# Kernel optimization log

Hardware: AMD Instinct MI355X
Metric: run time of the kernel (lower is better)

## Reference

```python
import jax, jax.numpy as jnp
import numpy as np

B, C, H, W = 4, 256, 64, 64
E = C // 8  # embedding_channels = inChannels // k


def setup_inputs() -> dict:
    key = jax.random.key(0)
    ks = jax.random.split(key, 9)
    sc = 1.0 / np.sqrt(C)
    so = 1.0 / np.sqrt(E)
    return {
        "x": jax.random.normal(ks[0], (B, C, H, W), dtype=jnp.float32),
        "Wk": jax.random.normal(ks[1], (E, C), dtype=jnp.float32) * sc,
        "bk": jax.random.normal(ks[2], (E,), dtype=jnp.float32) * 0.01,
        "Wq": jax.random.normal(ks[3], (E, C), dtype=jnp.float32) * sc,
        "bq": jax.random.normal(ks[4], (E,), dtype=jnp.float32) * 0.01,
        "Wv": jax.random.normal(ks[5], (E, C), dtype=jnp.float32) * sc,
        "bv": jax.random.normal(ks[6], (E,), dtype=jnp.float32) * 0.01,
        "Wo": jax.random.normal(ks[7], (C, E), dtype=jnp.float32) * so,
        "bo": jax.random.normal(ks[8], (C,), dtype=jnp.float32) * 0.01,
    }


def reference(x, Wk, bk, Wq, bq, Wv, bv, Wo, bo):
    b, c, h, w = x.shape
    n = h * w
    gamma = jnp.float32(0.5)  # non-learned branch (learned=False default)

    def conv1x1(inp, Wt, bt):
        # 1x1 conv == channel-mixing matmul: [b,c,h,w] x [e,c] -> [b,e,h,w]
        return jnp.einsum('bchw,ec->behw', inp, Wt) + bt[None, :, None, None]

    f = conv1x1(x, Wk, bk).reshape(b, -1, n)  # key   [b,E,N]
    g = conv1x1(x, Wq, bq).reshape(b, -1, n)  # query [b,E,N]
    hx = conv1x1(x, Wv, bv).reshape(b, -1, n)  # value [b,E,N]

    s = jnp.einsum('bei,bej->bij', f, g)       # f^T @ g, [b,N,N]
    beta = jax.nn.softmax(s, axis=1)           # softmax over dim 1 (rows) as in torch
    v = jnp.einsum('bei,bij->bej', hx, beta)   # h @ beta, [b,E,N]
    v = v.reshape(b, -1, h, w)

    o = jnp.einsum('behw,ce->bchw', v, Wo) + bo[None, :, None, None]
    y = gamma * o + x
    return y, o, gamma
```

## Files before the change

kernel.cpp:

```cpp
#include <hip/hip_runtime.h>

#define B_ 4
#define C_ 256
#define N_ 4096
#define E_ 32

typedef _Float16 f16x8 __attribute__((ext_vector_type(8)));
typedef _Float16 f16x4 __attribute__((ext_vector_type(4)));
typedef float f32x4 __attribute__((ext_vector_type(4)));

#define LOG2E 1.44269504088896f

#define XSWZ(row, col) ((col) ^ ((((row) >> 2) & 7) << 3))

__global__ __launch_bounds__(256) void proj_kernel(
    const float* __restrict__ x,
    const float* __restrict__ Wk, const float* __restrict__ bk,
    const float* __restrict__ Wq, const float* __restrict__ bq,
    const float* __restrict__ Wv, const float* __restrict__ bv,
    const float* __restrict__ Wo,
    _Float16* __restrict__ Qb, _Float16* __restrict__ Kb, _Float16* __restrict__ Vb,
    _Float16* __restrict__ Wof16, float* __restrict__ out)
{
    const int m = blockIdx.x >> 8;
    if (m == 3) {
        for (int i4 = threadIdx.x; i4 < (C_ * E_) / 4; i4 += 256) {
            float4 wv = ((const float4*)Wo)[i4];
            f16x4 tp = {(_Float16)wv.x, (_Float16)wv.y, (_Float16)wv.z, (_Float16)wv.w};
            *(f16x4*)&Wof16[i4 * 4] = tp;
        }
        if (threadIdx.x == 0)
            out[(size_t)2 * B_ * C_ * N_] = 0.5f;
        return;
    }
    const int rem = blockIdx.x & 255;
    const int b   = rem >> 6;
    const int n0  = (rem & 63) << 6;
    const int t    = threadIdx.x;
    const int lane = t & 63;
    const int wave = t >> 6;
    const int l15  = lane & 15;
    const int quad = lane >> 4;

    __shared__ _Float16 xT[64][264];
    __shared__ _Float16 Wl[32][264];

    const float* W    = (m == 0) ? Wk : (m == 1) ? Wq : Wv;
    const float* bias = (m == 0) ? bk : (m == 1) ? bq : bv;

    for (int i4 = t; i4 < (E_ * C_) / 4; i4 += 256) {
        float4 wv = ((const float4*)W)[i4];
        int e = (i4 * 4) >> 8, c = (i4 * 4) & 255;
        f16x4 tp = {(_Float16)wv.x, (_Float16)wv.y, (_Float16)wv.z, (_Float16)wv.w};
        *(f16x4*)&Wl[e][c] = tp;
    }
    for (int i4 = t; i4 < (64 * 256) / 4; i4 += 256) {
        int j4 = (i4 & 15) * 4;
        int c  = i4 >> 4;
        float4 xv = *(const float4*)(x + (size_t)(b * C_ + c) * N_ + n0 + j4);
        xT[j4 + 0][XSWZ(j4 + 0, c)] = (_Float16)xv.x;
        xT[j4 + 1][XSWZ(j4 + 1, c)] = (_Float16)xv.y;
        xT[j4 + 2][XSWZ(j4 + 2, c)] = (_Float16)xv.z;
        xT[j4 + 3][XSWZ(j4 + 3, c)] = (_Float16)xv.w;
    }
    __syncthreads();

    const int row = wave * 16 + l15;
    f16x8 Bf[8];
    for (int kk = 0; kk < 8; ++kk)
        Bf[kk] = *(const f16x8*)&xT[row][XSWZ(row, kk * 32 + quad * 8)];

    const float sc = (m == 1) ? LOG2E : 1.0f;
    for (int et = 0; et < 2; ++et) {
        f32x4 acc = {0.f, 0.f, 0.f, 0.f};
        for (int kk = 0; kk < 8; ++kk) {
            f16x8 Af = *(const f16x8*)&Wl[et * 16 + l15][kk * 32 + quad * 8];
            acc = __builtin_amdgcn_mfma_f32_16x16x32_f16(Af, Bf[kk], acc, 0, 0, 0);
        }
        const int n  = n0 + wave * 16 + l15;
        const int e0 = et * 16 + quad * 4;
        if (m == 2) {
            for (int r = 0; r < 4; ++r)
                Vb[(size_t)(b * E_ + e0 + r) * N_ + n] =
                    (_Float16)(acc[r] + bias[e0 + r]);
        } else {
            f16x4 st;
            for (int r = 0; r < 4; ++r)
                st[r] = (_Float16)((acc[r] + bias[e0 + r]) * sc);
            _Float16* dst = (m == 0) ? Kb : Qb;
            *(f16x4*)&dst[(size_t)(b * N_ + n) * E_ + e0] = st;
        }
    }
}

__global__ __launch_bounds__(512, 6) void attn_kernel(
    const _Float16* __restrict__ Qb, const _Float16* __restrict__ Kb,
    const _Float16* __restrict__ Vb, const _Float16* __restrict__ Wof16,
    const float* __restrict__ bo, const float* __restrict__ x,
    float* __restrict__ out)
{
    const int wave = threadIdx.x >> 6;
    const int lane = threadIdx.x & 63;
    const int l15  = lane & 15, quad = lane >> 4;
    const int jg   = blockIdx.x;
    const int b    = jg >> 8;
    const int j0   = (jg & 255) << 4;

    __shared__ __align__(16) char pbuf[8][2176];
    __shared__ float    mls[8][2][16];
    __shared__ _Float16 Om[16][40];

    _Float16 (*pb)[40] = (_Float16 (*)[40])(pbuf[wave]);

    f16x8 Qf = *(const f16x8*)(Qb + (size_t)(b * N_ + j0 + l15) * E_ + quad * 8);

    f32x4 O0 = {0, 0, 0, 0}, O1 = {0, 0, 0, 0};
    float mrow = -1e30f, lsum = 0.f;

    const _Float16* Kp = Kb + (size_t)b * N_ * E_ + (size_t)(wave << 9) * E_;
    const _Float16* Vp = Vb + (size_t)b * E_ * N_ + (wave << 9);

    f16x8 K0 = *(const f16x8*)(Kp + (size_t)l15 * E_ + quad * 8);
    f16x8 K1 = *(const f16x8*)(Kp + (size_t)(16 + l15) * E_ + quad * 8);
    f16x8 Va = *(const f16x8*)(Vp + (size_t)l15 * N_ + quad * 8);
    f16x8 Vc = *(const f16x8*)(Vp + (size_t)(16 + l15) * N_ + quad * 8);

    for (int it = 0; it < 16; ++it) {
        f32x4 z = {0, 0, 0, 0};
        f32x4 S0 = __builtin_amdgcn_mfma_f32_16x16x32_f16(K0, Qf, z, 0, 0, 0);
        f32x4 S1 = __builtin_amdgcn_mfma_f32_16x16x32_f16(K1, Qf, z, 0, 0, 0);
        const int i0n = ((it + 1) & 15) << 5;
        K0 = *(const f16x8*)(Kp + (size_t)(i0n + l15) * E_ + quad * 8);
        K1 = *(const f16x8*)(Kp + (size_t)(i0n + 16 + l15) * E_ + quad * 8);

        float mx = fmaxf(fmaxf(fmaxf(S0[0], S0[1]), fmaxf(S0[2], S0[3])),
                         fmaxf(fmaxf(S1[0], S1[1]), fmaxf(S1[2], S1[3])));
        mx = fmaxf(mx, __shfl_xor(mx, 16));
        mx = fmaxf(mx, __shfl_xor(mx, 32));
        if (__any(mx > mrow + 8.f)) {
            float mnew  = fmaxf(mrow, mx);
            float alpha = exp2f(mrow - mnew);
            mrow = mnew;
            lsum *= alpha;
            O0 *= alpha;
            O1 *= alpha;
        }
        float p00 = exp2f(S0[0] - mrow), p01 = exp2f(S0[1] - mrow);
        float p02 = exp2f(S0[2] - mrow), p03 = exp2f(S0[3] - mrow);
        float p10 = exp2f(S1[0] - mrow), p11 = exp2f(S1[1] - mrow);
        float p12 = exp2f(S1[2] - mrow), p13 = exp2f(S1[3] - mrow);
        lsum += ((p00 + p01) + (p02 + p03)) + ((p10 + p11) + (p12 + p13));

        f16x4 w0 = {(_Float16)p00, (_Float16)p01, (_Float16)p02, (_Float16)p03};
        f16x4 w1 = {(_Float16)p10, (_Float16)p11, (_Float16)p12, (_Float16)p13};
        *(f16x4*)&pb[l15][quad * 4]      = w0;
        *(f16x4*)&pb[l15][16 + quad * 4] = w1;
        f16x8 P = *(const f16x8*)&pb[l15][quad * 8];

        O0 = __builtin_amdgcn_mfma_f32_16x16x32_f16(Va, P, O0, 0, 0, 0);
        O1 = __builtin_amdgcn_mfma_f32_16x16x32_f16(Vc, P, O1, 0, 0, 0);
        Va = *(const f16x8*)(Vp + (size_t)l15 * N_ + i0n + quad * 8);
        Vc = *(const f16x8*)(Vp + (size_t)(16 + l15) * N_ + i0n + quad * 8);
    }

    lsum += __shfl_xor(lsum, 16);
    lsum += __shfl_xor(lsum, 32);
    if (quad == 0) { mls[wave][0][l15] = mrow; mls[wave][1][l15] = lsum; }
    __syncthreads();

    float M = -1e30f, ms[8], ls[8];
    for (int s = 0; s < 8; ++s) {
        ms[s] = mls[s][0][l15]; ls[s] = mls[s][1][l15];
        M = fmaxf(M, ms[s]);
    }
    float L = 0.f;
    for (int s = 0; s < 8; ++s) L += ls[s] * exp2f(ms[s] - M);
    const float w = exp2f(mrow - M) / L;

    float (*osum)[34] = (float (*)[34])(pbuf[wave]);
    *(f32x4*)&osum[l15][quad * 4]      = O0 * w;
    *(f32x4*)&osum[l15][16 + quad * 4] = O1 * w;
    __syncthreads();

    {
        const int j = threadIdx.x >> 5;
        const int e = threadIdx.x & 31;
        float a = 0.f;
        for (int s = 0; s < 8; ++s)
            a += ((const float (*)[34])(pbuf[s]))[j][e];
        Om[j][e] = (_Float16)a;
    }
    __syncthreads();

    f16x8 Bf2 = *(const f16x8*)&Om[l15][quad * 8];
    float* out_y = out + (size_t)b * C_ * N_;
    float* out_o = out + (size_t)B_ * C_ * N_ + (size_t)b * C_ * N_;
    const float* xb = x + (size_t)b * C_ * N_;
    for (int ct = 0; ct < 2; ++ct) {
        const int c0 = wave * 32 + ct * 16;
        f16x8 Af = *(const f16x8*)(Wof16 + (size_t)(c0 + l15) * E_ + quad * 8);
        f32x4 z = {0, 0, 0, 0};
        f32x4 acc = __builtin_amdgcn_mfma_f32_16x16x32_f16(Af, Bf2, z, 0, 0, 0);
        for (int r = 0; r < 4; ++r) {
            const int c = c0 + quad * 4 + r;
            size_t idx = (size_t)c * N_ + j0 + l15;
            float ov = acc[r] + bo[c];
            out_o[idx] = ov;
            out_y[idx] = 0.5f * ov + xb[idx];
        }
    }
}

extern "C" void kernel_launch(void* const* d_in, const int* in_sizes, int n_in,
                              void* d_out, int out_size, void* d_ws, size_t ws_size,
                              hipStream_t stream)
{
    const float* x  = (const float*)d_in[0];
    const float* Wk = (const float*)d_in[1];
    const float* bk = (const float*)d_in[2];
    const float* Wq = (const float*)d_in[3];
    const float* bq = (const float*)d_in[4];
    const float* Wv = (const float*)d_in[5];
    const float* bv = (const float*)d_in[6];
    const float* Wo = (const float*)d_in[7];
    const float* bo = (const float*)d_in[8];
    float* out = (float*)d_out;

    char* ws = (char*)d_ws;
    _Float16* Qb    = (_Float16*)(ws);
    _Float16* Kb    = (_Float16*)(ws + (1u << 20));
    _Float16* Vb    = (_Float16*)(ws + (2u << 20));
    _Float16* Wof16 = (_Float16*)(ws + (3u << 20));

    proj_kernel<<<dim3(3 * B_ * (N_ / 64) + 1), dim3(256), 0, stream>>>(
        x, Wk, bk, Wq, bq, Wv, bv, Wo, Qb, Kb, Vb, Wof16, out);
    attn_kernel<<<dim3(B_ * (N_ / 16)), dim3(512), 0, stream>>>(
        Qb, Kb, Vb, Wof16, bo, x, out);
}
```

Measured before the change: 145.7 us.

## Process four query tiles per attention block and fuse QKV projections per tile

The attention kernel now handles 64 query columns per block (four 16-wide sub-tiles), so each K/V fragment loaded from global memory is reused across four query tiles. This cuts K/V traffic by a factor of four at the cost of more registers, so launch bounds drop to 2 blocks per SM. The projection kernel computes K, Q and V in one block per x tile, so x is loaded and converted once instead of three times. V is also written in a blocked layout through LDS so the attention loads are contiguous.

```diff
diff --git a/kernel.cpp b/kernel.cpp
--- a/kernel.cpp
+++ b/kernel.cpp
@@ -19,11 +19,10 @@
     const float* __restrict__ Wq, const float* __restrict__ bq,
     const float* __restrict__ Wv, const float* __restrict__ bv,
     const float* __restrict__ Wo,
-    _Float16* __restrict__ Qb, _Float16* __restrict__ Kb, _Float16* __restrict__ Vb,
+    _Float16* __restrict__ Qb, _Float16* __restrict__ Kb, _Float16* __restrict__ Vt,
     _Float16* __restrict__ Wof16, float* __restrict__ out)
 {
-    const int m = blockIdx.x >> 8;
-    if (m == 3) {
+    if (blockIdx.x == 256) {
         for (int i4 = threadIdx.x; i4 < (C_ * E_) / 4; i4 += 256) {
             float4 wv = ((const float4*)Wo)[i4];
             f16x4 tp = {(_Float16)wv.x, (_Float16)wv.y, (_Float16)wv.z, (_Float16)wv.w};
@@ -33,9 +32,8 @@
             out[(size_t)2 * B_ * C_ * N_] = 0.5f;
         return;
     }
-    const int rem = blockIdx.x & 255;
-    const int b   = rem >> 6;
-    const int n0  = (rem & 63) << 6;
+    const int b  = blockIdx.x >> 6;
+    const int n0 = (blockIdx.x & 63) << 6;
     const int t    = threadIdx.x;
     const int lane = t & 63;
     const int wave = t >> 6;
@@ -44,16 +42,8 @@
 
     __shared__ _Float16 xT[64][264];
     __shared__ _Float16 Wl[32][264];
-
-    const float* W    = (m == 0) ? Wk : (m == 1) ? Wq : Wv;
-    const float* bias = (m == 0) ? bk : (m == 1) ? bq : bv;
-
-    for (int i4 = t; i4 < (E_ * C_) / 4; i4 += 256) {
-        float4 wv = ((const float4*)W)[i4];
-        int e = (i4 * 4) >> 8, c = (i4 * 4) & 255;
-        f16x4 tp = {(_Float16)wv.x, (_Float16)wv.y, (_Float16)wv.z, (_Float16)wv.w};
-        *(f16x4*)&Wl[e][c] = tp;
-    }
+    __shared__ _Float16 vT[32][72];
+
     for (int i4 = t; i4 < (64 * 256) / 4; i4 += 256) {
         int j4 = (i4 & 15) * 4;
         int c  = i4 >> 4;
@@ -63,39 +53,68 @@
         xT[j4 + 2][XSWZ(j4 + 2, c)] = (_Float16)xv.z;
         xT[j4 + 3][XSWZ(j4 + 3, c)] = (_Float16)xv.w;
     }
-    __syncthreads();
+
+    const float* Ws[3] = {Wk, Wq, Wv};
+    const float* bs[3] = {bk, bq, bv};
 
     const int row = wave * 16 + l15;
     f16x8 Bf[8];
-    for (int kk = 0; kk < 8; ++kk)
-        Bf[kk] = *(const f16x8*)&xT[row][XSWZ(row, kk * 32 + quad * 8)];
-
-    const float sc = (m == 1) ? LOG2E : 1.0f;
-    for (int et = 0; et < 2; ++et) {
-        f32x4 acc = {0.f, 0.f, 0.f, 0.f};
-        for (int kk = 0; kk < 8; ++kk) {
-            f16x8 Af = *(const f16x8*)&Wl[et * 16 + l15][kk * 32 + quad * 8];
-            acc = __builtin_amdgcn_mfma_f32_16x16x32_f16(Af, Bf[kk], acc, 0, 0, 0);
-        }
-        const int n  = n0 + wave * 16 + l15;
-        const int e0 = et * 16 + quad * 4;
-        if (m == 2) {
-            for (int r = 0; r < 4; ++r)
-                Vb[(size_t)(b * E_ + e0 + r) * N_ + n] =
-                    (_Float16)(acc[r] + bias[e0 + r]);
-        } else {
-            f16x4 st;
-            for (int r = 0; r < 4; ++r)
-                st[r] = (_Float16)((acc[r] + bias[e0 + r]) * sc);
-            _Float16* dst = (m == 0) ? Kb : Qb;
-            *(f16x4*)&dst[(size_t)(b * N_ + n) * E_ + e0] = st;
-        }
+
+    for (int m = 0; m < 3; ++m) {
+        for (int i4 = t; i4 < (E_ * C_) / 4; i4 += 256) {
+            float4 wv = ((const float4*)Ws[m])[i4];
+            int e = (i4 * 4) >> 8, c = (i4 * 4) & 255;
+            f16x4 tp = {(_Float16)wv.x, (_Float16)wv.y, (_Float16)wv.z, (_Float16)wv.w};
+            *(f16x4*)&Wl[e][XSWZ(e, c)] = tp;
+        }
+        __syncthreads();
+        if (m == 0) {
+            #pragma unroll
+            for (int kk = 0; kk < 8; ++kk)
+                Bf[kk] = *(const f16x8*)&xT[row][XSWZ(row, kk * 32 + quad * 8)];
+        }
+        const float sc = (m == 1) ? LOG2E : 1.0f;
+        const float* bias = bs[m];
+        #pragma unroll
+        for (int et = 0; et < 2; ++et) {
+            f32x4 acc = {0.f, 0.f, 0.f, 0.f};
+            #pragma unroll
+            for (int kk = 0; kk < 8; ++kk) {
+                const int e = et * 16 + l15;
+                f16x8 Af = *(const f16x8*)&Wl[e][XSWZ(e, kk * 32 + quad * 8)];
+                acc = __builtin_amdgcn_mfma_f32_16x16x32_f16(Af, Bf[kk], acc, 0, 0, 0);
+            }
+            const int n  = n0 + wave * 16 + l15;
+            const int e0 = et * 16 + quad * 4;
+            if (m == 2) {
+                #pragma unroll
+                for (int r = 0; r < 4; ++r)
+                    vT[e0 + r][wave * 16 + l15] = (_Float16)(acc[r] + bias[e0 + r]);
+            } else {
+                f16x4 st;
+                #pragma unroll
+                for (int r = 0; r < 4; ++r)
+                    st[r] = (_Float16)((acc[r] + bias[e0 + r]) * sc);
+                _Float16* dst = (m == 0) ? Kb : Qb;
+                *(f16x4*)&dst[(size_t)(b * N_ + n) * E_ + e0] = st;
+            }
+        }
+        __syncthreads();
+    }
+
+    {
+        const int e_s = t >> 3;
+        const int nb  = t & 7;
+        f16x8 v = *(const f16x8*)&vT[e_s][nb * 8];
+        size_t base = ((size_t)(b * 128 + (n0 >> 5) + (nb >> 2)) * 32 + e_s) * 32
+                    + (nb & 3) * 8;
+        *(f16x8*)&Vt[base] = v;
     }
 }
 
-__global__ __launch_bounds__(512, 6) void attn_kernel(
+__global__ __launch_bounds__(512, 2) void attn_kernel(
     const _Float16* __restrict__ Qb, const _Float16* __restrict__ Kb,
-    const _Float16* __restrict__ Vb, const _Float16* __restrict__ Wof16,
+    const _Float16* __restrict__ Vt, const _Float16* __restrict__ Wof16,
     const float* __restrict__ bo, const float* __restrict__ x,
     float* __restrict__ out)
 {
@@ -103,110 +122,150 @@
     const int lane = threadIdx.x & 63;
     const int l15  = lane & 15, quad = lane >> 4;
     const int jg   = blockIdx.x;
-    const int b    = jg >> 8;
-    const int j0   = (jg & 255) << 4;
-
-    __shared__ __align__(16) char pbuf[8][2176];
-    __shared__ float    mls[8][2][16];
-    __shared__ _Float16 Om[16][40];
-
-    _Float16 (*pb)[40] = (_Float16 (*)[40])(pbuf[wave]);
-
-    f16x8 Qf = *(const f16x8*)(Qb + (size_t)(b * N_ + j0 + l15) * E_ + quad * 8);
-
-    f32x4 O0 = {0, 0, 0, 0}, O1 = {0, 0, 0, 0};
-    float mrow = -1e30f, lsum = 0.f;
+    const int b    = jg >> 6;
+    const int j0   = (jg & 63) << 6;
+
+    __shared__ __align__(16) char big[8][4][2176];
+    __shared__ float    mls[8][2][4][16];
+    __shared__ _Float16 Om[4][16][40];
+
+    _Float16 (*pb)[40] = (_Float16 (*)[40])(big[wave][0]);
+
+    f16x8 Qf[4];
+    #pragma unroll
+    for (int cc = 0; cc < 4; ++cc)
+        Qf[cc] = *(const f16x8*)(Qb + (size_t)(b * N_ + j0 + cc * 16 + l15) * E_ + quad * 8);
+
+    f32x4 O0c[4], O1c[4];
+    float mrow[4], lsum[4];
+    #pragma unroll
+    for (int cc = 0; cc < 4; ++cc) {
+        O0c[cc] = (f32x4){0, 0, 0, 0}; O1c[cc] = (f32x4){0, 0, 0, 0};
+        mrow[cc] = -1e30f; lsum[cc] = 0.f;
+    }
 
     const _Float16* Kp = Kb + (size_t)b * N_ * E_ + (size_t)(wave << 9) * E_;
-    const _Float16* Vp = Vb + (size_t)b * E_ * N_ + (wave << 9);
+    const _Float16* Vp = Vt + ((size_t)(b * 128 + wave * 16) << 10);
 
     f16x8 K0 = *(const f16x8*)(Kp + (size_t)l15 * E_ + quad * 8);
     f16x8 K1 = *(const f16x8*)(Kp + (size_t)(16 + l15) * E_ + quad * 8);
-    f16x8 Va = *(const f16x8*)(Vp + (size_t)l15 * N_ + quad * 8);
-    f16x8 Vc = *(const f16x8*)(Vp + (size_t)(16 + l15) * N_ + quad * 8);
+    f16x8 Va = *(const f16x8*)(Vp + l15 * 32 + quad * 8);
+    f16x8 Vc = *(const f16x8*)(Vp + (16 + l15) * 32 + quad * 8);
 
     for (int it = 0; it < 16; ++it) {
+        const int i0n = ((it + 1) & 15) << 5;
+        f32x4 S0[4], S1[4];
         f32x4 z = {0, 0, 0, 0};
-        f32x4 S0 = __builtin_amdgcn_mfma_f32_16x16x32_f16(K0, Qf, z, 0, 0, 0);
-        f32x4 S1 = __builtin_amdgcn_mfma_f32_16x16x32_f16(K1, Qf, z, 0, 0, 0);
-        const int i0n = ((it + 1) & 15) << 5;
+        #pragma unroll
+        for (int cc = 0; cc < 4; ++cc) {
+            S0[cc] = __builtin_amdgcn_mfma_f32_16x16x32_f16(K0, Qf[cc], z, 0, 0, 0);
+            S1[cc] = __builtin_amdgcn_mfma_f32_16x16x32_f16(K1, Qf[cc], z, 0, 0, 0);
+        }
         K0 = *(const f16x8*)(Kp + (size_t)(i0n + l15) * E_ + quad * 8);
         K1 = *(const f16x8*)(Kp + (size_t)(i0n + 16 + l15) * E_ + quad * 8);
 
-        float mx = fmaxf(fmaxf(fmaxf(S0[0], S0[1]), fmaxf(S0[2], S0[3])),
-                         fmaxf(fmaxf(S1[0], S1[1]), fmaxf(S1[2], S1[3])));
-        mx = fmaxf(mx, __shfl_xor(mx, 16));
-        mx = fmaxf(mx, __shfl_xor(mx, 32));
-        if (__any(mx > mrow + 8.f)) {
-            float mnew  = fmaxf(mrow, mx);
-            float alpha = exp2f(mrow - mnew);
-            mrow = mnew;
-            lsum *= alpha;
-            O0 *= alpha;
-            O1 *= alpha;
-        }
-        float p00 = exp2f(S0[0] - mrow), p01 = exp2f(S0[1] - mrow);
-        float p02 = exp2f(S0[2] - mrow), p03 = exp2f(S0[3] - mrow);
-        float p10 = exp2f(S1[0] - mrow), p11 = exp2f(S1[1] - mrow);
-        float p12 = exp2f(S1[2] - mrow), p13 = exp2f(S1[3] - mrow);
-        lsum += ((p00 + p01) + (p02 + p03)) + ((p10 + p11) + (p12 + p13));
-
-        f16x4 w0 = {(_Float16)p00, (_Float16)p01, (_Float16)p02, (_Float16)p03};
-        f16x4 w1 = {(_Float16)p10, (_Float16)p11, (_Float16)p12, (_Float16)p13};
-        *(f16x4*)&pb[l15][quad * 4]      = w0;
-        *(f16x4*)&pb[l15][16 + quad * 4] = w1;
-        f16x8 P = *(const f16x8*)&pb[l15][quad * 8];
-
-        O0 = __builtin_amdgcn_mfma_f32_16x16x32_f16(Va, P, O0, 0, 0, 0);
-        O1 = __builtin_amdgcn_mfma_f32_16x16x32_f16(Vc, P, O1, 0, 0, 0);
-        Va = *(const f16x8*)(Vp + (size_t)l15 * N_ + i0n + quad * 8);
-        Vc = *(const f16x8*)(Vp + (size_t)(16 + l15) * N_ + i0n + quad * 8);
-    }
-
-    lsum += __shfl_xor(lsum, 16);
-    lsum += __shfl_xor(lsum, 32);
-    if (quad == 0) { mls[wave][0][l15] = mrow; mls[wave][1][l15] = lsum; }
+        #pragma unroll
+        for (int cc = 0; cc < 4; ++cc) {
+            float mx = fmaxf(
+                fmaxf(fmaxf(S0[cc][0], S0[cc][1]), fmaxf(S0[cc][2], S0[cc][3])),
+                fmaxf(fmaxf(S1[cc][0], S1[cc][1]), fmaxf(S1[cc][2], S1[cc][3])));
+            mx = fmaxf(mx, __shfl_xor(mx, 16));
+            mx = fmaxf(mx, __shfl_xor(mx, 32));
+            if (__any(mx > mrow[cc] + 8.f)) {
+                float mnew  = fmaxf(mrow[cc], mx);
+                float alpha = exp2f(mrow[cc] - mnew);
+                mrow[cc] = mnew;
+                lsum[cc] *= alpha;
+                O0c[cc] *= alpha;
+                O1c[cc] *= alpha;
+            }
+            float m0 = mrow[cc];
+            float p00 = exp2f(S0[cc][0] - m0), p01 = exp2f(S0[cc][1] - m0);
+            float p02 = exp2f(S0[cc][2] - m0), p03 = exp2f(S0[cc][3] - m0);
+            float p10 = exp2f(S1[cc][0] - m0), p11 = exp2f(S1[cc][1] - m0);
+            float p12 = exp2f(S1[cc][2] - m0), p13 = exp2f(S1[cc][3] - m0);
+            lsum[cc] += ((p00 + p01) + (p02 + p03)) + ((p10 + p11) + (p12 + p13));
+
+            f16x4 w0 = {(_Float16)p00, (_Float16)p01, (_Float16)p02, (_Float16)p03};
+            f16x4 w1 = {(_Float16)p10, (_Float16)p11, (_Float16)p12, (_Float16)p13};
+            *(f16x4*)&pb[l15][quad * 4]      = w0;
+            *(f16x4*)&pb[l15][16 + quad * 4] = w1;
+            f16x8 P = *(const f16x8*)&pb[l15][quad * 8];
+
+            O0c[cc] = __builtin_amdgcn_mfma_f32_16x16x32_f16(Va, P, O0c[cc], 0, 0, 0);
+            O1c[cc] = __builtin_amdgcn_mfma_f32_16x16x32_f16(Vc, P, O1c[cc], 0, 0, 0);
+        }
+        Va = *(const f16x8*)(Vp + (i0n << 5) + l15 * 32 + quad * 8);
+        Vc = *(const f16x8*)(Vp + (i0n << 5) + (16 + l15) * 32 + quad * 8);
+    }
+
+    #pragma unroll
+    for (int cc = 0; cc < 4; ++cc) {
+        float ls = lsum[cc];
+        ls += __shfl_xor(ls, 16);
+        ls += __shfl_xor(ls, 32);
+        if (quad == 0) { mls[wave][0][cc][l15] = mrow[cc]; mls[wave][1][cc][l15] = ls; }
+    }
     __syncthreads();
 
-    float M = -1e30f, ms[8], ls[8];
-    for (int s = 0; s < 8; ++s) {
-        ms[s] = mls[s][0][l15]; ls[s] = mls[s][1][l15];
-        M = fmaxf(M, ms[s]);
-    }
-    float L = 0.f;
-    for (int s = 0; s < 8; ++s) L += ls[s] * exp2f(ms[s] - M);
-    const float w = exp2f(mrow - M) / L;
-
-    float (*osum)[34] = (float (*)[34])(pbuf[wave]);
-    *(f32x4*)&osum[l15][quad * 4]      = O0 * w;
-    *(f32x4*)&osum[l15][16 + quad * 4] = O1 * w;
+    #pragma unroll
+    for (int cc = 0; cc < 4; ++cc) {
+        float M = -1e30f, ms[8], ls[8];
+        #pragma unroll
+        for (int s = 0; s < 8; ++s) {
+            ms[s] = mls[s][0][cc][l15]; ls[s] = mls[s][1][cc][l15];
+            M = fmaxf(M, ms[s]);
+        }
+        float L = 0.f;
+        #pragma unroll
+        for (int s = 0; s < 8; ++s) L += ls[s] * exp2f(ms[s] - M);
+        const float w = exp2f(mrow[cc] - M) / L;
+        float (*osum)[34] = (float (*)[34])(big[wave][cc]);
+        *(f32x4*)&osum[l15][quad * 4]      = O0c[cc] * w;
+        *(f32x4*)&osum[l15][16 + quad * 4] = O1c[cc] * w;
+    }
     __syncthreads();
 
     {
         const int j = threadIdx.x >> 5;
         const int e = threadIdx.x & 31;
-        float a = 0.f;
-        for (int s = 0; s < 8; ++s)
-            a += ((const float (*)[34])(pbuf[s]))[j][e];
-        Om[j][e] = (_Float16)a;
+        #pragma unroll
+        for (int cc = 0; cc < 4; ++cc) {
+            float a = 0.f;
+            #pragma unroll
+            for (int s = 0; s < 8; ++s)
+                a += ((const float (*)[34])(big[s][cc]))[j][e];
+            Om[cc][j][e] = (_Float16)a;
+        }
     }
     __syncthreads();
 
-    f16x8 Bf2 = *(const f16x8*)&Om[l15][quad * 8];
+    f16x8 Bf2[4];
+    #pragma unroll
+    for (int cc = 0; cc < 4; ++cc)
+        Bf2[cc] = *(const f16x8*)&Om[cc][l15][quad * 8];
     float* out_y = out + (size_t)b * C_ * N_;
     float* out_o = out + (size_t)B_ * C_ * N_ + (size_t)b * C_ * N_;
     const float* xb = x + (size_t)b * C_ * N_;
+    #pragma unroll
     for (int ct = 0; ct < 2; ++ct) {
         const int c0 = wave * 32 + ct * 16;
         f16x8 Af = *(const f16x8*)(Wof16 + (size_t)(c0 + l15) * E_ + quad * 8);
+        f32x4 acc[4];
         f32x4 z = {0, 0, 0, 0};
-        f32x4 acc = __builtin_amdgcn_mfma_f32_16x16x32_f16(Af, Bf2, z, 0, 0, 0);
+        #pragma unroll
+        for (int cc = 0; cc < 4; ++cc)
+            acc[cc] = __builtin_amdgcn_mfma_f32_16x16x32_f16(Af, Bf2[cc], z, 0, 0, 0);
+        #pragma unroll
         for (int r = 0; r < 4; ++r) {
             const int c = c0 + quad * 4 + r;
-            size_t idx = (size_t)c * N_ + j0 + l15;
-            float ov = acc[r] + bo[c];
-            out_o[idx] = ov;
-            out_y[idx] = 0.5f * ov + xb[idx];
+            #pragma unroll
+            for (int cc = 0; cc < 4; ++cc) {
+                size_t idx = (size_t)c * N_ + j0 + cc * 16 + l15;
+                float ov = acc[cc][r] + bo[c];
+                out_o[idx] = ov;
+                out_y[idx] = 0.5f * ov + xb[idx];
+            }
         }
     }
 }
@@ -229,11 +288,11 @@
     char* ws = (char*)d_ws;
     _Float16* Qb    = (_Float16*)(ws);
     _Float16* Kb    = (_Float16*)(ws + (1u << 20));
-    _Float16* Vb    = (_Float16*)(ws + (2u << 20));
+    _Float16* Vt    = (_Float16*)(ws + (2u << 20));
     _Float16* Wof16 = (_Float16*)(ws + (3u << 20));
 
-    proj_kernel<<<dim3(3 * B_ * (N_ / 64) + 1), dim3(256), 0, stream>>>(
-        x, Wk, bk, Wq, bq, Wv, bv, Wo, Qb, Kb, Vb, Wof16, out);
-    attn_kernel<<<dim3(B_ * (N_ / 16)), dim3(512), 0, stream>>>(
-        Qb, Kb, Vb, Wof16, bo, x, out);
+    proj_kernel<<<dim3(257), dim3(256), 0, stream>>>(
+        x, Wk, bk, Wq, bq, Wv, bv, Wo, Qb, Kb, Vt, Wof16, out);
+    attn_kernel<<<dim3(B_ * (N_ / 64)), dim3(512), 0, stream>>>(
+        Qb, Kb, Vt, Wof16, bo, x, out);
 }
```

Result: faster. 136.9 us (-6.0%).
